# Optimization experiments

Hardware: AMD Instinct MI355X
Metric: run time of the kernel (lower is better)

The kernel has to match this reference:

```python
import jax, jax.numpy as jnp
import numpy as np

N_NODES = 50000
N_EDGES = 1600000
D = 128
N_GRAPHS = 512


def _glorot(key, shape):
    fan_in, fan_out = shape[1], shape[0]
    lim = float(np.sqrt(6.0 / (fan_in + fan_out)))
    return jax.random.uniform(key, shape, jnp.float32, -lim, lim)


def setup_inputs() -> dict:
    key = jax.random.key(0)
    ks = jax.random.split(key, 16)
    inp = {
        "x": jax.random.normal(ks[0], (N_NODES, D), jnp.float32),
        "edge_index": jax.random.randint(ks[1], (2, N_EDGES), 0, N_NODES, jnp.int64),
        "batch": jnp.sort(jax.random.randint(ks[2], (N_NODES,), 0, N_GRAPHS, jnp.int64)),
    }
    # 3 SAGEConv layers: W_l (neighbor path, with bias), W_r (root path, no bias)
    for l in range(3):
        inp[f"Wl{l}"] = _glorot(ks[3 + 3 * l], (D, D))
        inp[f"b{l}"] = jnp.zeros((D,), jnp.float32)
        inp[f"Wr{l}"] = _glorot(ks[4 + 3 * l], (D, D))
    inp["fc_w"] = _glorot(ks[14], (1, D))
    inp["fc_b"] = jnp.zeros((1,), jnp.float32)
    return inp


def _sage_layer(x, src, dst, Wl, b, Wr):
    # mean aggregation of source features at destination nodes
    deg = jax.ops.segment_sum(jnp.ones((src.shape[0],), x.dtype), dst, num_segments=N_NODES)
    agg = jax.ops.segment_sum(x[src], dst, num_segments=N_NODES)  # [N, D] gather+scatter
    agg = agg / jnp.clip(deg, 1.0)[:, None]
    return agg @ Wl.T + b + x @ Wr.T


def reference(x, edge_index, batch, Wl0, b0, Wr0, Wl1, b1, Wr1, Wl2, b2, Wr2, fc_w, fc_b):
    src, dst = edge_index[0], edge_index[1]
    for Wl, b, Wr in ((Wl0, b0, Wr0), (Wl1, b1, Wr1), (Wl2, b2, Wr2)):
        x = jax.nn.relu(_sage_layer(x, src, dst, Wl, b, Wr))  # dropout p=0 -> identity
    # global mean pool per graph
    cnt = jax.ops.segment_sum(jnp.ones((x.shape[0],), x.dtype), batch, num_segments=N_GRAPHS)
    pooled = jax.ops.segment_sum(x, batch, num_segments=N_GRAPHS) / jnp.clip(cnt, 1.0)[:, None]
    return pooled @ fc_w.T + fc_b
```

## Files before the change

### kernel.cpp

```cpp
#include <hip/hip_runtime.h>

#define N_NODES  50000
#define N_EDGES  1600000
#define DIM      128
#define N_GRAPHS 512
#define SCAN_BLOCK 1024
#define NB1   196
#define B1    256
#define CHUNK 6250
#define BH_N  (NB1 * B1)
#define BH_BLK ((BH_N + SCAN_BLOCK - 1) / SCAN_BLOCK)
#define XS_BLOCKS 6250
#define WS_BLOCKS 384
#define GB_BLOCKS 196
#define OI_BLOCKS 2

typedef unsigned int uint_t;
typedef unsigned short ushort_t;
typedef __attribute__((ext_vector_type(8))) short bf16x8;
typedef __attribute__((ext_vector_type(4))) float f32x4;

__device__ inline uint_t bf_rne(float f) {
    uint_t u = __float_as_uint(f);
    return (u + 0x7fffu + ((u >> 16) & 1u)) >> 16;
}

__device__ inline void bf_split(float f, uint_t& h, uint_t& l) {
    h = bf_rne(f);
    float hf = __uint_as_float(h << 16);
    l = bf_rne(f - hf);
}

__global__ __launch_bounds__(256) void prep_kernel(
        const int* __restrict__ dst, int* __restrict__ bh,
        const float* __restrict__ x, ushort_t* __restrict__ xh, ushort_t* __restrict__ xl,
        const float* w0, const float* w1, const float* w2,
        const float* w3, const float* w4, const float* w5,
        ushort_t* __restrict__ whi,
        const int* __restrict__ batch, int* __restrict__ gstart,
        const float* __restrict__ fc_b, float* __restrict__ out) {
    __shared__ int hist[NB1];
    int b = blockIdx.x, t = threadIdx.x;
    if (b < B1) {
        for (int i = t; i < NB1; i += 256) hist[i] = 0;
        __syncthreads();
        int base = b * CHUNK;
        for (int i = t; i < CHUNK; i += 256)
            atomicAdd(&hist[dst[base + i] >> 8], 1);
        __syncthreads();
        for (int i = t; i < NB1; i += 256) bh[i * B1 + b] = hist[i];
    } else if (b < B1 + XS_BLOCKS) {
        int i = (b - B1) * 256 + t;
        float4 v = ((const float4*)x)[i];
        uint_t h0,h1,h2,h3,l0,l1,l2,l3;
        bf_split(v.x,h0,l0); bf_split(v.y,h1,l1); bf_split(v.z,h2,l2); bf_split(v.w,h3,l3);
        uint2 ho; ho.x = h0 | (h1 << 16); ho.y = h2 | (h3 << 16);
        uint2 lo; lo.x = l0 | (l1 << 16); lo.y = l2 | (l3 << 16);
        ((uint2*)xh)[i] = ho;
        ((uint2*)xl)[i] = lo;
    } else if (b < B1 + XS_BLOCKS + WS_BLOCKS) {
        int i = (b - B1 - XS_BLOCKS) * 256 + t;
        int ws = i >> 14, off = i & 16383;
        const float* w = (ws == 0) ? w0 : (ws == 1) ? w1 : (ws == 2) ? w2
                       : (ws == 3) ? w3 : (ws == 4) ? w4 : w5;
        whi[i] = (ushort_t)bf_rne(w[off]);
    } else if (b < B1 + XS_BLOCKS + WS_BLOCKS + GB_BLOCKS) {
        int i = (b - B1 - XS_BLOCKS - WS_BLOCKS) * 256 + t;
        if (i < N_NODES) {
            int bb = batch[i];
            int prev = (i == 0) ? -1 : batch[i - 1];
            for (int g = prev + 1; g <= bb; g++) gstart[g] = i;
            if (i == 0) {
                int last = batch[N_NODES - 1];
                for (int g = last + 1; g <= N_GRAPHS; g++) gstart[g] = N_NODES;
            }
        }
    } else {
        int i = (b - B1 - XS_BLOCKS - WS_BLOCKS - GB_BLOCKS) * 256 + t;
        if (i < N_GRAPHS) out[i] = fc_b[0];
    }
}

__global__ void block_reduce_n(const int* __restrict__ in, int* __restrict__ bsum, int n) {
    __shared__ int red[256];
    int b = blockIdx.x, t = threadIdx.x;
    int base = b * SCAN_BLOCK;
    int s = 0;
    for (int i = t; i < SCAN_BLOCK; i += 256) {
        int idx = base + i;
        s += (idx < n) ? in[idx] : 0;
    }
    red[t] = s; __syncthreads();
    for (int off = 128; off; off >>= 1) {
        if (t < off) red[t] += red[t + off];
        __syncthreads();
    }
    if (t == 0) bsum[b] = red[0];
}

__global__ void scan_finalize(const int* __restrict__ in, const int* __restrict__ bsum,
                              int* __restrict__ ofs, int n, int nblk) {
    __shared__ int small[64];
    __shared__ int tmp[SCAN_BLOCK];
    int b = blockIdx.x, t = threadIdx.x;
    if (t < 64) {
        int v = (t < nblk) ? bsum[t] : 0;
        for (int off = 1; off < 64; off <<= 1) {
            int u = __shfl_up(v, off, 64);
            if (t >= off) v += u;
        }
        small[t] = v;
    }
    __syncthreads();
    int base = (b == 0) ? 0 : small[b - 1];
    int i = b * SCAN_BLOCK + t;
    tmp[t] = (i < n) ? in[i] : 0;
    __syncthreads();
    for (int off = 1; off < SCAN_BLOCK; off <<= 1) {
        int add = (t >= off) ? tmp[t - off] : 0;
        __syncthreads();
        tmp[t] += add;
        __syncthreads();
    }
    if (i < n) ofs[i + 1] = tmp[t] + base;
    if (i == 0) ofs[0] = 0;
}

__global__ __launch_bounds__(256) void p1_scatter(const int* __restrict__ src,
                                                  const int* __restrict__ dst,
                                                  const int* __restrict__ bhofs,
                                                  uint_t* __restrict__ ebuf1) {
    __shared__ int cur[NB1];
    int b = blockIdx.x, t = threadIdx.x;
    for (int i = t; i < NB1; i += 256) cur[i] = bhofs[i * B1 + b];
    __syncthreads();
    int base = b * CHUNK;
    for (int i = t; i < CHUNK; i += 256) {
        int d = dst[base + i];
        int pos = atomicAdd(&cur[d >> 8], 1);
        ebuf1[pos] = (uint_t)src[base + i] | ((uint_t)(d & 255) << 16);
    }
}

__global__ __launch_bounds__(256) void p2_sort(const uint_t* __restrict__ ebuf1,
                                               const int* __restrict__ bhofs,
                                               int* __restrict__ row_start,
                                               int* __restrict__ ebuf) {
    __shared__ int hist[256];
    __shared__ int scn[256];
    __shared__ int cur[256];
    int k = blockIdx.x, t = threadIdx.x;
    int s = bhofs[k * B1];
    int e = (k == NB1 - 1) ? N_EDGES : bhofs[(k + 1) * B1];
    hist[t] = 0;
    __syncthreads();
    for (int i = s + t; i < e; i += 256)
        atomicAdd(&hist[(ebuf1[i] >> 16) & 255], 1);
    __syncthreads();
    int v = hist[t];
    scn[t] = v;
    __syncthreads();
    for (int off = 1; off < 256; off <<= 1) {
        int add = (t >= off) ? scn[t - off] : 0;
        __syncthreads();
        scn[t] += add;
        __syncthreads();
    }
    int ex = scn[t] - v;
    int node = k * 256 + t;
    if (node < N_NODES) row_start[node] = s + ex;
    if (k == NB1 - 1 && t == 0) row_start[N_NODES] = N_EDGES;
    cur[t] = s + ex;
    __syncthreads();
    for (int i = s + t; i < e; i += 256) {
        uint_t p = ebuf1[i];
        int pos = atomicAdd(&cur[(p >> 16) & 255], 1);
        ebuf[pos] = (int)(p & 0xffffu);
    }
}

__global__ __launch_bounds__(256) void agg_kernel(const ushort_t* __restrict__ xb,
                                                  const int* __restrict__ row_start,
                                                  const int* __restrict__ ebuf,
                                                  ushort_t* __restrict__ agg_hi,
                                                  ushort_t* __restrict__ agg_lo) {
    int node = blockIdx.x * 4 + (threadIdx.x >> 6);
    if (node >= N_NODES) return;
    int lane = threadIdx.x & 63;
    int grp = lane >> 4, fl = lane & 15;
    int s = row_start[node], e = row_start[node + 1];
    float a0=0.f,a1=0.f,a2=0.f,a3=0.f,a4=0.f,a5=0.f,a6=0.f,a7=0.f;
    const uint4* x8 = (const uint4*)xb;
    for (int i = s; i < e; i += 64) {
        int nloc = e - i; if (nloc > 64) nloc = 64;
        int src_l = (i + lane < e) ? ebuf[i + lane] : 0;
        int jmax = (nloc + 3) & ~3;
        #pragma unroll 4
        for (int j = 0; j < jmax; j += 4) {
            int slot = j + grp;
            int src = __shfl(src_l, slot & 63, 64);
            if (slot < nloc) {
                uint4 v = x8[(size_t)src * 16 + fl];
                a0 += __uint_as_float(v.x << 16);
                a1 += __uint_as_float(v.x & 0xffff0000u);
                a2 += __uint_as_float(v.y << 16);
                a3 += __uint_as_float(v.y & 0xffff0000u);
                a4 += __uint_as_float(v.z << 16);
                a5 += __uint_as_float(v.z & 0xffff0000u);
                a6 += __uint_as_float(v.w << 16);
                a7 += __uint_as_float(v.w & 0xffff0000u);
            }
        }
    }
    a0 += __shfl_xor(a0, 16, 64); a0 += __shfl_xor(a0, 32, 64);
    a1 += __shfl_xor(a1, 16, 64); a1 += __shfl_xor(a1, 32, 64);
    a2 += __shfl_xor(a2, 16, 64); a2 += __shfl_xor(a2, 32, 64);
    a3 += __shfl_xor(a3, 16, 64); a3 += __shfl_xor(a3, 32, 64);
    a4 += __shfl_xor(a4, 16, 64); a4 += __shfl_xor(a4, 32, 64);
    a5 += __shfl_xor(a5, 16, 64); a5 += __shfl_xor(a5, 32, 64);
    a6 += __shfl_xor(a6, 16, 64); a6 += __shfl_xor(a6, 32, 64);
    a7 += __shfl_xor(a7, 16, 64); a7 += __shfl_xor(a7, 32, 64);
    if (grp == 0) {
        float inv = (e > s) ? 1.0f / (float)(e - s) : 0.0f;
        float v[8] = {a0*inv,a1*inv,a2*inv,a3*inv,a4*inv,a5*inv,a6*inv,a7*inv};
        uint_t h[8], l[8];
        #pragma unroll
        for (int k = 0; k < 8; k++) bf_split(v[k], h[k], l[k]);
        uint4 ho, lo;
        ho.x = h[0] | (h[1] << 16); ho.y = h[2] | (h[3] << 16);
        ho.z = h[4] | (h[5] << 16); ho.w = h[6] | (h[7] << 16);
        lo.x = l[0] | (l[1] << 16); lo.y = l[2] | (l[3] << 16);
        lo.z = l[4] | (l[5] << 16); lo.w = l[6] | (l[7] << 16);
        ((uint4*)agg_hi)[(size_t)node * 16 + fl] = ho;
        ((uint4*)agg_lo)[(size_t)node * 16 + fl] = lo;
    }
}

__global__ __launch_bounds__(256, 2) void sage_gemm_mfma(
        const ushort_t* __restrict__ agg_hi, const ushort_t* __restrict__ agg_lo,
        const ushort_t* __restrict__ x_hi,   const ushort_t* __restrict__ x_lo,
        const ushort_t* __restrict__ wl_hi,  const ushort_t* __restrict__ wr_hi,
        const float* __restrict__ bias,
        ushort_t* __restrict__ out_hi, ushort_t* __restrict__ out_lo,
        const int* __restrict__ batch, const int* __restrict__ gstart,
        const float* __restrict__ fc_w, float* __restrict__ pool_out, int nrows) {
    __shared__ ushort_t whi_s[2][16384];
    __shared__ float pool_red[64];
    int t = threadIdx.x;
    for (int i = t; i < 4096; i += 256) {
        int a = i >> 11, rem = i & 2047, row = rem >> 4, ch = rem & 15;
        int sw = ch ^ (row & 7);
        const ushort_t* srcp = a ? wr_hi : wl_hi;
        uint4 v = *(const uint4*)(srcp + row * DIM + ch * 8);
        *(uint4*)((char*)&whi_s[a][0] + row * 256 + sw * 16) = v;
    }
    __syncthreads();

    int wave = t >> 6, lane = t & 63;
    int ml = lane & 15, quad = lane >> 4;
    int m0 = blockIdx.x * 64 + wave * 16;
    int row = m0 + ml;
    int rowc = (row < nrows) ? row : (nrows - 1);
    size_t abase = (size_t)rowc * DIM + quad * 8;

    f32x4 acc[8];
    #pragma unroll
    for (int i = 0; i < 8; i++) acc[i] = (f32x4)0.f;

    #pragma unroll
    for (int kc = 0; kc < DIM; kc += 32) {
        bf16x8 Aah = *(const bf16x8*)(agg_hi + abase + kc);
        bf16x8 Aal = *(const bf16x8*)(agg_lo + abase + kc);
        bf16x8 Axh = *(const bf16x8*)(x_hi   + abase + kc);
        bf16x8 Axl = *(const bf16x8*)(x_lo   + abase + kc);
        int kch = (kc >> 3) + quad;
        int sw16 = (kch ^ (ml & 7)) * 16;
        #pragma unroll
        for (int n0 = 0; n0 < 8; n0++) {
            int nrow = n0 * 16 + ml;
            bf16x8 b_lh = *(const bf16x8*)((const char*)&whi_s[0][0] + nrow * 256 + sw16);
            bf16x8 b_rh = *(const bf16x8*)((const char*)&whi_s[1][0] + nrow * 256 + sw16);
            f32x4 c = acc[n0];
            c = __builtin_amdgcn_mfma_f32_16x16x32_bf16(Aah, b_lh, c, 0, 0, 0);
            c = __builtin_amdgcn_mfma_f32_16x16x32_bf16(Aal, b_lh, c, 0, 0, 0);
            c = __builtin_amdgcn_mfma_f32_16x16x32_bf16(Axh, b_rh, c, 0, 0, 0);
            c = __builtin_amdgcn_mfma_f32_16x16x32_bf16(Axl, b_rh, c, 0, 0, 0);
            acc[n0] = c;
        }
    }

    if (pool_out) {
        float rd[4] = {0.f, 0.f, 0.f, 0.f};
        #pragma unroll
        for (int n0 = 0; n0 < 8; n0++) {
            int col = n0 * 16 + ml;
            float bv = bias[col];
            float w  = fc_w[col];
            #pragma unroll
            for (int r = 0; r < 4; r++)
                rd[r] += fmaxf(acc[n0][r] + bv, 0.f) * w;
        }
        #pragma unroll
        for (int r = 0; r < 4; r++) {
            #pragma unroll
            for (int off = 1; off < 16; off <<= 1)
                rd[r] += __shfl_xor(rd[r], off, 64);
        }
        if (ml == 0) {
            #pragma unroll
            for (int r = 0; r < 4; r++)
                pool_red[wave * 16 + quad * 4 + r] = rd[r];
        }
        __syncthreads();
        if (wave == 0) {
            int grow = blockIdx.x * 64 + lane;
            int valid = grow < nrows;
            int g = valid ? batch[grow] : 0;
            float v = 0.f;
            if (valid) v = pool_red[lane] / (float)(gstart[g + 1] - gstart[g]);
            int lastrow = blockIdx.x * 64 + 63;
            if (lastrow > nrows - 1) lastrow = nrows - 1;
            int g0 = batch[blockIdx.x * 64];
            int g1 = batch[lastrow];
            for (int gg = g0; gg <= g1; gg++) {
                float part = (valid && g == gg) ? v : 0.f;
                #pragma unroll
                for (int off = 1; off < 64; off <<= 1)
                    part += __shfl_xor(part, off, 64);
                if (lane == 0) atomicAdd(&pool_out[gg], part);
            }
        }
    } else {
        #pragma unroll
        for (int n0 = 0; n0 < 8; n0++) {
            int col = n0 * 16 + ml;
            float bv = bias[col];
            #pragma unroll
            for (int r = 0; r < 4; r++) {
                int orow = m0 + quad * 4 + r;
                if (orow < nrows) {
                    float v = fmaxf(acc[n0][r] + bv, 0.f);
                    uint_t h, l;
                    bf_split(v, h, l);
                    out_hi[(size_t)orow * DIM + col] = (ushort_t)h;
                    out_lo[(size_t)orow * DIM + col] = (ushort_t)l;
                }
            }
        }
    }
}

extern "C" void kernel_launch(void* const* d_in, const int* in_sizes, int n_in,
                              void* d_out, int out_size, void* d_ws, size_t ws_size,
                              hipStream_t stream) {
    const float* x     = (const float*)d_in[0];
    const int*   ei    = (const int*)d_in[1];
    const int*   batch = (const int*)d_in[2];
    const float* Wl[3] = {(const float*)d_in[3], (const float*)d_in[6], (const float*)d_in[9]};
    const float* bb[3] = {(const float*)d_in[4], (const float*)d_in[7], (const float*)d_in[10]};
    const float* Wr[3] = {(const float*)d_in[5], (const float*)d_in[8], (const float*)d_in[11]};
    const float* fc_w  = (const float*)d_in[12];
    const float* fc_b  = (const float*)d_in[13];
    float* out = (float*)d_out;

    char* p = (char*)d_ws;
    auto alloc = [&](size_t bytes) { char* r = p; p += (bytes + 255) & ~255ull; return r; };
    int* bh        = (int*)alloc((size_t)BH_N * 4);
    int* bhofs     = (int*)alloc((size_t)(BH_N + 1) * 4);
    int* bsum      = (int*)alloc((size_t)BH_BLK * 4);
    uint_t* ebuf1  = (uint_t*)alloc((size_t)N_EDGES * 4);
    int* ebuf      = (int*)alloc((size_t)N_EDGES * 4);
    int* row_start = (int*)alloc((size_t)(N_NODES + 1) * 4);
    int* gstart    = (int*)alloc((size_t)(N_GRAPHS + 1) * 4);
    const size_t FB = (size_t)N_NODES * DIM * 2;
    ushort_t* agg_hi = (ushort_t*)alloc(FB);
    ushort_t* agg_lo = (ushort_t*)alloc(FB);
    ushort_t* fh[3]  = {(ushort_t*)alloc(FB), (ushort_t*)alloc(FB), (ushort_t*)alloc(FB)};
    ushort_t* fl_[3] = {(ushort_t*)alloc(FB), (ushort_t*)alloc(FB), (ushort_t*)alloc(FB)};
    ushort_t* whi    = (ushort_t*)alloc((size_t)6 * 16384 * 2);

    const int* src = ei;
    const int* dst = ei + N_EDGES;

    prep_kernel<<<B1 + XS_BLOCKS + WS_BLOCKS + GB_BLOCKS + OI_BLOCKS, 256, 0, stream>>>(
        dst, bh, x, fh[0], fl_[0], Wl[0], Wr[0], Wl[1], Wr[1], Wl[2], Wr[2],
        whi, batch, gstart, fc_b, out);
    block_reduce_n<<<BH_BLK, 256, 0, stream>>>(bh, bsum, BH_N);
    scan_finalize<<<BH_BLK, SCAN_BLOCK, 0, stream>>>(bh, bsum, bhofs, BH_N, BH_BLK);
    p1_scatter<<<B1, 256, 0, stream>>>(src, dst, bhofs, ebuf1);
    p2_sort<<<NB1, 256, 0, stream>>>(ebuf1, bhofs, row_start, ebuf);

    int inb = 0;
    for (int l = 0; l < 3; l++) {
        int outb = (l == 0) ? 1 : 2;
        agg_kernel<<<(N_NODES + 3) / 4, 256, 0, stream>>>(fh[inb], row_start, ebuf, agg_hi, agg_lo);
        sage_gemm_mfma<<<(N_NODES + 63) / 64, 256, 0, stream>>>(
            agg_hi, agg_lo, fh[inb], fl_[inb],
            whi + (size_t)(2 * l) * 16384, whi + (size_t)(2 * l + 1) * 16384,
            bb[l], fh[outb], fl_[outb],
            batch, gstart, fc_w, (l == 2) ? out : (float*)nullptr, N_NODES);
        inb = outb;
    }
}
```

Baseline: 392.3 us.

## Fold bucket-histogram scan into scatter and sort kernels, dropping two launches

Removes the separate block-reduce and scan-finalize kernels. p1_scatter now recomputes its per-bucket offsets by having each thread sum one 256-entry row of the histogram, then doing a shared-memory scan across rows. p2_sort recomputes its bucket start and end with block reductions over the histogram prefix. This trades two kernel launches and their serialization for redundant histogram reads (each p1 thread reads 256 ints, and p2 blocks read up to 50K ints), with more scan work repeated in every block.

Result: slower. 408.1 us (+4.0%).

```diff
diff --git a/kernel.cpp b/kernel.cpp
--- a/kernel.cpp
+++ b/kernel.cpp
@@ -4,12 +4,10 @@
 #define N_EDGES  1600000
 #define DIM      128
 #define N_GRAPHS 512
-#define SCAN_BLOCK 1024
 #define NB1   196
 #define B1    256
 #define CHUNK 6250
 #define BH_N  (NB1 * B1)
-#define BH_BLK ((BH_N + SCAN_BLOCK - 1) / SCAN_BLOCK)
 #define XS_BLOCKS 6250
 #define WS_BLOCKS 384
 #define GB_BLOCKS 196
@@ -81,58 +79,32 @@
     }
 }
 
-__global__ void block_reduce_n(const int* __restrict__ in, int* __restrict__ bsum, int n) {
-    __shared__ int red[256];
-    int b = blockIdx.x, t = threadIdx.x;
-    int base = b * SCAN_BLOCK;
-    int s = 0;
-    for (int i = t; i < SCAN_BLOCK; i += 256) {
-        int idx = base + i;
-        s += (idx < n) ? in[idx] : 0;
-    }
-    red[t] = s; __syncthreads();
-    for (int off = 128; off; off >>= 1) {
-        if (t < off) red[t] += red[t + off];
-        __syncthreads();
-    }
-    if (t == 0) bsum[b] = red[0];
-}
-
-__global__ void scan_finalize(const int* __restrict__ in, const int* __restrict__ bsum,
-                              int* __restrict__ ofs, int n, int nblk) {
-    __shared__ int small[64];
-    __shared__ int tmp[SCAN_BLOCK];
-    int b = blockIdx.x, t = threadIdx.x;
-    if (t < 64) {
-        int v = (t < nblk) ? bsum[t] : 0;
-        for (int off = 1; off < 64; off <<= 1) {
-            int u = __shfl_up(v, off, 64);
-            if (t >= off) v += u;
-        }
-        small[t] = v;
-    }
-    __syncthreads();
-    int base = (b == 0) ? 0 : small[b - 1];
-    int i = b * SCAN_BLOCK + t;
-    tmp[t] = (i < n) ? in[i] : 0;
-    __syncthreads();
-    for (int off = 1; off < SCAN_BLOCK; off <<= 1) {
-        int add = (t >= off) ? tmp[t - off] : 0;
-        __syncthreads();
-        tmp[t] += add;
-        __syncthreads();
-    }
-    if (i < n) ofs[i + 1] = tmp[t] + base;
-    if (i == 0) ofs[0] = 0;
-}
-
 __global__ __launch_bounds__(256) void p1_scatter(const int* __restrict__ src,
                                                   const int* __restrict__ dst,
-                                                  const int* __restrict__ bhofs,
+                                                  const int* __restrict__ bh,
                                                   uint_t* __restrict__ ebuf1) {
+    __shared__ int rowscan[256];
     __shared__ int cur[NB1];
     int b = blockIdx.x, t = threadIdx.x;
-    for (int i = t; i < NB1; i += 256) cur[i] = bhofs[i * B1 + b];
+    int rs = 0, ps = 0;
+    if (t < NB1) {
+        const int* row = bh + t * B1;
+        for (int c = 0; c < B1; c++) {
+            int v = row[c];
+            rs += v;
+            if (c < b) ps += v;
+        }
+    }
+    rowscan[t] = rs;
+    __syncthreads();
+    int own = rs;
+    for (int off = 1; off < 256; off <<= 1) {
+        int add = (t >= off) ? rowscan[t - off] : 0;
+        __syncthreads();
+        rowscan[t] += add;
+        __syncthreads();
+    }
+    if (t < NB1) cur[t] = (rowscan[t] - own) + ps;
     __syncthreads();
     int base = b * CHUNK;
     for (int i = t; i < CHUNK; i += 256) {
@@ -143,15 +115,36 @@
 }
 
 __global__ __launch_bounds__(256) void p2_sort(const uint_t* __restrict__ ebuf1,
-                                               const int* __restrict__ bhofs,
+                                               const int* __restrict__ bh,
                                                int* __restrict__ row_start,
                                                int* __restrict__ ebuf) {
+    __shared__ int red[256];
+    __shared__ int s_sh, e_sh;
     __shared__ int hist[256];
     __shared__ int scn[256];
     __shared__ int cur[256];
     int k = blockIdx.x, t = threadIdx.x;
-    int s = bhofs[k * B1];
-    int e = (k == NB1 - 1) ? N_EDGES : bhofs[(k + 1) * B1];
+    int acc = 0;
+    int limit = k * B1;
+    for (int i = t; i < limit; i += 256) acc += bh[i];
+    red[t] = acc;
+    __syncthreads();
+    for (int off = 128; off; off >>= 1) {
+        if (t < off) red[t] += red[t + off];
+        __syncthreads();
+    }
+    if (t == 0) s_sh = red[0];
+    __syncthreads();
+    red[t] = bh[k * B1 + t];
+    __syncthreads();
+    for (int off = 128; off; off >>= 1) {
+        if (t < off) red[t] += red[t + off];
+        __syncthreads();
+    }
+    if (t == 0) e_sh = s_sh + red[0];
+    __syncthreads();
+    int s = s_sh, e = e_sh;
+
     hist[t] = 0;
     __syncthreads();
     for (int i = s + t; i < e; i += 256)
@@ -366,8 +359,6 @@
     char* p = (char*)d_ws;
     auto alloc = [&](size_t bytes) { char* r = p; p += (bytes + 255) & ~255ull; return r; };
     int* bh        = (int*)alloc((size_t)BH_N * 4);
-    int* bhofs     = (int*)alloc((size_t)(BH_N + 1) * 4);
-    int* bsum      = (int*)alloc((size_t)BH_BLK * 4);
     uint_t* ebuf1  = (uint_t*)alloc((size_t)N_EDGES * 4);
     int* ebuf      = (int*)alloc((size_t)N_EDGES * 4);
     int* row_start = (int*)alloc((size_t)(N_NODES + 1) * 4);
@@ -385,10 +376,8 @@
     prep_kernel<<<B1 + XS_BLOCKS + WS_BLOCKS + GB_BLOCKS + OI_BLOCKS, 256, 0, stream>>>(
         dst, bh, x, fh[0], fl_[0], Wl[0], Wr[0], Wl[1], Wr[1], Wl[2], Wr[2],
         whi, batch, gstart, fc_b, out);
-    block_reduce_n<<<BH_BLK, 256, 0, stream>>>(bh, bsum, BH_N);
-    scan_finalize<<<BH_BLK, SCAN_BLOCK, 0, stream>>>(bh, bsum, bhofs, BH_N, BH_BLK);
-    p1_scatter<<<B1, 256, 0, stream>>>(src, dst, bhofs, ebuf1);
-    p2_sort<<<NB1, 256, 0, stream>>>(ebuf1, bhofs, row_start, ebuf);
+    p1_scatter<<<B1, 256, 0, stream>>>(src, dst, bh, ebuf1);
+    p2_sort<<<NB1, 256, 0, stream>>>(ebuf1, bh, row_start, ebuf);
 
     int inb = 0;
     for (int l = 0; l < 3; l++) {
```
